# Optimization experiments

Hardware: AMD Instinct MI355X
Metric: run time of the kernel (lower is better)

## Reference

```python
import jax, jax.numpy as jnp
import numpy as np

K = 7            # kernel_size
PAD = 3          # (dilation*(K-1)+1)//2
SHARE = 8        # share_planes
CIN = 512; REL = 64; COUT = 512
B = 4; H = 32; W = 32
EPS = 1e-5


def _patches(x, k, pad):
    """Reflect-pad then extract kxk local windows.
    x: [B,C,H,W] -> [B, C, k*k, H*W] (row-major kernel-offset ordering,
    matching torch Unfold / SAN's Subtraction ordering)."""
    b, c, h, w = x.shape
    xp = jnp.pad(x, ((0, 0), (0, 0), (pad, pad), (pad, pad)), mode='reflect')
    pats = jnp.stack([xp[:, :, i:i + h, j:j + w]
                      for i in range(k) for j in range(k)], axis=2)
    return pats.reshape(b, c, k * k, h * w)


def setup_inputs() -> dict:
    key = jax.random.key(0)
    ks = jax.random.split(key, 16)
    n = lambda k_, shp, s=0.05: jax.random.normal(k_, shp, dtype=jnp.float32) * s
    return {
        'x': jax.random.normal(ks[0], (B, CIN, H, W), dtype=jnp.float32),
        # 1x1 query/key/value projections
        'w1': n(ks[1], (REL, CIN)), 'b1': n(ks[2], (REL,)),
        'w2': n(ks[3], (REL, CIN)), 'b2': n(ks[4], (REL,)),
        'w3': n(ks[5], (COUT, CIN)), 'b3': n(ks[6], (COUT,)),
        # conv_p: 1x1 conv on 2-channel position map
        'wp': n(ks[7], (2, 2), 0.5), 'bp': n(ks[8], (2,)),
        # conv_w: BN(rel+2) -> ReLU -> 1x1(rel+2->rel, no bias) -> BN(rel) -> ReLU -> 1x1(rel->out/share)
        'g0': jnp.ones((REL + 2,), jnp.float32), 'be0': jnp.zeros((REL + 2,), jnp.float32),
        'm0': n(ks[9], (REL + 2,), 0.1),
        'v0': jax.random.uniform(ks[10], (REL + 2,), jnp.float32, 0.5, 1.5),
        'wcw1': n(ks[11], (REL, REL + 2)),
        'g1': jnp.ones((REL,), jnp.float32), 'be1': jnp.zeros((REL,), jnp.float32),
        'm1': n(ks[12], (REL,), 0.1),
        'v1': jax.random.uniform(ks[13], (REL,), jnp.float32, 0.5, 1.5),
        'wcw2': n(ks[14], (COUT // SHARE, REL)), 'bcw2': n(ks[15], (COUT // SHARE,)),
    }


def reference(x, w1, b1, w2, b2, w3, b3, wp, bp,
              g0, be0, m0, v0, wcw1, g1, be1, m1, v1, wcw2, bcw2):
    b, c, h, w = x.shape
    hw = h * w
    conv1x1 = lambda W_, B_, t: jnp.einsum('oc,bchw->bohw', W_, t) + B_[None, :, None, None]
    bn = lambda t, g, be, m, v: ((t - m[None, :, None, None])
                                 * (g * jax.lax.rsqrt(v + EPS))[None, :, None, None]
                                 + be[None, :, None, None])

    x1 = conv1x1(w1, b1, x)   # [B,REL,H,W]
    x2 = conv1x1(w2, b2, x)   # [B,REL,H,W]
    x3 = conv1x1(w3, b3, x)   # [B,COUT,H,W]

    # position map: channel 0 = loc_w, channel 1 = loc_h (as in source)
    lw = jnp.broadcast_to(jnp.linspace(-1.0, 1.0, w)[None, :], (h, w))
    lh = jnp.broadcast_to(jnp.linspace(-1.0, 1.0, h)[:, None], (h, w))
    p = jnp.stack([lw, lh])[None].astype(x.dtype)          # [1,2,H,W]
    p = jnp.einsum('oc,bchw->bohw', wp, p) + bp[None, :, None, None]

    # Subtraction2(x1, x2): center query minus key neighbors -> [B,REL,K*K,HW]
    sub2 = x1.reshape(b, REL, 1, hw) - _patches(x2, K, PAD)
    # Subtraction(p): center minus neighbors -> [1,2,K*K,HW], repeat over batch
    subp = p.reshape(1, 2, 1, hw) - _patches(p, K, PAD)
    subp = jnp.broadcast_to(subp, (b, 2, K * K, hw))

    t = jnp.concatenate([sub2, subp], axis=1)              # [B,REL+2,K*K,HW]
    t = jax.nn.relu(bn(t, g0, be0, m0, v0))
    t = jnp.einsum('oc,bckn->bokn', wcw1, t)               # [B,REL,K*K,HW]
    t = jax.nn.relu(bn(t, g1, be1, m1, v1))
    wgt = jnp.einsum('oc,bckn->bokn', wcw2, t) + bcw2[None, :, None, None]
    wgt = jax.nn.softmax(wgt, axis=-2)                     # softmax over K*K window dim

    # Aggregation: out[b,c,n] = sum_k wgt[b, c//SHARE, k, n] * x3_patch[b,c,k,n]
    x3p = _patches(x3, K, PAD).reshape(b, COUT // SHARE, SHARE, K * K, hw)
    out = jnp.einsum('bgskn,bgkn->bgsn', x3p, wgt)
    return out.reshape(b, COUT, h, w)
```

## Files before the change

### kernel.cpp

```cpp
#include <hip/hip_runtime.h>
#include <hip/hip_bf16.h>
#include <math.h>

typedef float f32x4 __attribute__((ext_vector_type(4)));
typedef short s16x8 __attribute__((ext_vector_type(8)));

#define KKW 49
#define HWTOT 1024
#define CIN 512
#define COUT 512

#define OFF_X1T 0
#define OFF_X2T 262144
#define OFF_X3T 524288
#define OFF_PM  2621440
#define OFF_A0  2623488
#define OFF_C0  2623554
#define OFF_W64 2623620
#define OFF_W65 2623684
#define OFF_C1V 2623748
#define OFF_W1B 2623812
#define OFF_W2B 2625860
#define OFF_W2F 2627908
#define OFF_WT  2629956
#define OFF_XT  2793796
#define WS_NEED_FLOATS 3842372ull

#define SWZ(bb)  ((bb) ^ ((((bb) >> 7) & 7) << 4))

#define GLD16(g, l) __builtin_amdgcn_global_load_lds( \
    (const __attribute__((address_space(1))) void*)(g), \
    (__attribute__((address_space(3))) void*)(l), 16, 0, 0)

__device__ __forceinline__ int refl(int m) {
    if (m < 0) m = -m;
    if (m > 31) m = 62 - m;
    return m;
}

__device__ __forceinline__ unsigned short fbf(float f) {
    unsigned u = __builtin_bit_cast(unsigned, f);
    unsigned r = u + 0x7fffu + ((u >> 16) & 1u);
    return (unsigned short)(r >> 16);
}

__device__ __forceinline__ unsigned pk2bf(float a, float b) {
    float2 f2; f2.x = a; f2.y = b;
    __hip_bfloat162 h = __float22bfloat162_rn(f2);
    union { __hip_bfloat162 h2; unsigned u; } cv;
    cv.h2 = h;
    return cv.u;
}

__device__ __forceinline__ float bf2f(unsigned short u) {
    unsigned v = (unsigned)u << 16;
    return __builtin_bit_cast(float, v);
}

__device__ __forceinline__ void setup_body(
        int tid,
        const float* __restrict__ wp, const float* __restrict__ bp,
        const float* __restrict__ g0, const float* __restrict__ be0,
        const float* __restrict__ m0, const float* __restrict__ v0,
        const float* __restrict__ wcw1,
        const float* __restrict__ g1, const float* __restrict__ be1,
        const float* __restrict__ m1, const float* __restrict__ v1,
        const float* __restrict__ wcw2,
        float* __restrict__ ws) {
    float* pm = ws + OFF_PM;
    for (int n = tid; n < HWTOT; n += 256) {
        int xx = n & 31, yy = n >> 5;
        float lw = -1.f + (2.f / 31.f) * xx;
        float lh = -1.f + (2.f / 31.f) * yy;
        pm[n * 2 + 0] = wp[0] * lw + wp[1] * lh + bp[0];
        pm[n * 2 + 1] = wp[2] * lw + wp[3] * lh + bp[1];
    }
    if (tid < 66) {
        float a = g0[tid] * rsqrtf(v0[tid] + 1e-5f);
        ws[OFF_A0 + tid] = a;
        ws[OFF_C0 + tid] = be0[tid] - m0[tid] * a;
    }
    if (tid < 64) {
        float a1c = g1[tid] * rsqrtf(v1[tid] + 1e-5f);
        ws[OFF_W64 + tid] = a1c * wcw1[tid * 66 + 64];
        ws[OFF_W65 + tid] = a1c * wcw1[tid * 66 + 65];
        ws[OFF_C1V + tid] = be1[tid] - m1[tid] * a1c;
    }
    unsigned short* w1b = (unsigned short*)(ws + OFF_W1B);
    unsigned short* w2f = (unsigned short*)(ws + OFF_W2F);
    for (int t = tid; t < 4096; t += 256) {
        int co = t >> 6, r = t & 63;
        float a1c = g1[co] * rsqrtf(v1[co] + 1e-5f);
        w1b[t] = fbf(a1c * wcw1[co * 66 + r]);
        int j = t & 7, idx = t >> 3;
        int ft = idx >> 6, l = idx & 63;
        int gt = ft >> 1, ks2 = ft & 1;
        int g = (l & 15) + gt * 16;
        int c2 = ks2 * 32 + (l >> 4) * 8 + j;
        w2f[t] = fbf(wcw2[g * 64 + c2]);
    }
}

__global__ void k_setup(const float* __restrict__ wp, const float* __restrict__ bp,
                        const float* __restrict__ g0, const float* __restrict__ be0,
                        const float* __restrict__ m0, const float* __restrict__ v0,
                        const float* __restrict__ wcw1,
                        const float* __restrict__ g1, const float* __restrict__ be1,
                        const float* __restrict__ m1, const float* __restrict__ v1,
                        const float* __restrict__ wcw2,
                        float* __restrict__ ws) {
    setup_body(threadIdx.x, wp, bp, g0, be0, m0, v0, wcw1, g1, be1, m1, v1, wcw2, ws);
}

__global__ __launch_bounds__(256) void k_prep(
        const float* __restrict__ x,
        const float* __restrict__ w1, const float* __restrict__ w2,
        const float* __restrict__ w3,
        const float* __restrict__ wp, const float* __restrict__ bp,
        const float* __restrict__ g0, const float* __restrict__ be0,
        const float* __restrict__ m0, const float* __restrict__ v0,
        const float* __restrict__ wcw1,
        const float* __restrict__ g1, const float* __restrict__ be1,
        const float* __restrict__ m1, const float* __restrict__ v1,
        const float* __restrict__ wcw2,
        float* __restrict__ ws) {
    int bid = blockIdx.x;
    int tid = threadIdx.x;
    if (bid == 296) {
        setup_body(tid, wp, bp, g0, be0, m0, v0, wcw1, g1, be1, m1, v1, wcw2, ws);
    } else if (bid < 40) {
        int mT = bid / 8, kT = bid % 8;
        char* dst = (char*)(ws + OFF_WT) + (mT * 8 + kT) * 16384;
#pragma unroll
        for (int it = 0; it < 4; ++it) {
            int item = it * 256 + tid;
            int m = item >> 3, k8 = item & 7;
            int mg = mT * 128 + m;
            const float* src;
            if (mg < 64) src = w1 + mg * CIN;
            else if (mg < 128) src = w2 + (mg - 64) * CIN;
            else src = w3 + (mg - 128) * CIN;
            int k0 = kT * 64 + k8 * 8;
            s16x8 h;
#pragma unroll
            for (int i = 0; i < 8; i++) h[i] = (short)fbf(src[k0 + i]);
            *(s16x8*)(dst + SWZ(m * 128 + k8 * 16)) = h;
        }
    } else {
        __shared__ float lds[64 * 129];
        int t = bid - 40;
        int b = t >> 6, nT = (t >> 3) & 7, kT = t & 7;
        const float* src = x + (b * CIN + kT * 64) * HWTOT + nT * 128;
#pragma unroll
        for (int it = 0; it < 8; ++it) {
            int item = it * 256 + tid;
            int kk = item >> 5, n4 = item & 31;
            float4 v = *(const float4*)(src + kk * HWTOT + n4 * 4);
            float* d = &lds[kk * 129 + n4 * 4];
            d[0] = v.x; d[1] = v.y; d[2] = v.z; d[3] = v.w;
        }
        __syncthreads();
        char* dst = (char*)(ws + OFF_XT) + ((b * 8 + nT) * 8 + kT) * 16384;
#pragma unroll
        for (int it = 0; it < 4; ++it) {
            int item = it * 256 + tid;
            int n = item >> 3, k8 = item & 7;
            s16x8 h;
#pragma unroll
            for (int i = 0; i < 8; i++) h[i] = (short)fbf(lds[(k8 * 8 + i) * 129 + n]);
            *(s16x8*)(dst + SWZ(n * 128 + k8 * 16)) = h;
        }
    }
}

__global__ __launch_bounds__(256) void k_projm(
        const float* __restrict__ b1, const float* __restrict__ b2,
        const float* __restrict__ b3, float* __restrict__ ws) {
    __shared__ __align__(16) char smem[65536];
    int tid = threadIdx.x, lane = tid & 63, wv = tid >> 6;
    int lidx = lane & 15, q = lane >> 4;
    int mT = blockIdx.x, nT = blockIdx.y, b = blockIdx.z;
    int mh = wv >> 1, nh = wv & 1;
    const char* wtg = (const char*)(ws + OFF_WT) + mT * 8 * 16384;
    const char* xtg = (const char*)(ws + OFF_XT) + (b * 8 + nT) * 8 * 16384;

    f32x4 acc[4][4];
#pragma unroll
    for (int i = 0; i < 4; i++)
#pragma unroll
        for (int j = 0; j < 4; j++) acc[i][j] = (f32x4)0.f;

#define STAGE(kt, buf) do { \
        const char* ga_ = wtg + (kt) * 16384; \
        const char* gb_ = xtg + (kt) * 16384; \
        char* la_ = smem + (buf) * 32768; \
        char* lb_ = la_ + 16384; \
        _Pragma("unroll") \
        for (int c_ = 0; c_ < 4; c_++) { \
            GLD16(ga_ + c_ * 4096 + wv * 1024 + lane * 16, la_ + c_ * 4096 + wv * 1024); \
            GLD16(gb_ + c_ * 4096 + wv * 1024 + lane * 16, lb_ + c_ * 4096 + wv * 1024); \
        } \
    } while (0)

    STAGE(0, 0);
    __syncthreads();
    for (int kt = 0; kt < 8; kt++) {
        if (kt < 7) STAGE(kt + 1, (kt + 1) & 1);
        const char* la = smem + (kt & 1) * 32768;
        const char* lb = la + 16384;
#pragma unroll
        for (int ks = 0; ks < 2; ks++) {
            s16x8 af[4], bf[4];
            int kb = ks * 64 + q * 16;
#pragma unroll
            for (int f = 0; f < 4; f++) {
                int arow = mh * 64 + f * 16 + lidx;
                int brow = nh * 64 + f * 16 + lidx;
                af[f] = *(const s16x8*)(la + SWZ(arow * 128 + kb));
                bf[f] = *(const s16x8*)(lb + SWZ(brow * 128 + kb));
            }
#pragma unroll
            for (int mf = 0; mf < 4; mf++)
#pragma unroll
                for (int nf = 0; nf < 4; nf++)
                    acc[mf][nf] = __builtin_amdgcn_mfma_f32_16x16x32_bf16(
                        af[mf], bf[nf], acc[mf][nf], 0, 0, 0);
        }
        __syncthreads();
    }
#undef STAGE

    unsigned short* x1t = (unsigned short*)(ws + OFF_X1T);
    unsigned short* x2t = (unsigned short*)(ws + OFF_X2T);
    unsigned short* x3t = (unsigned short*)(ws + OFF_X3T);
#pragma unroll
    for (int mf = 0; mf < 4; mf++) {
        int mloc = mh * 64 + mf * 16 + q * 4;
        int mg = mT * 128 + mloc;
#pragma unroll
        for (int nf = 0; nf < 4; nf++) {
            int n = nT * 128 + nh * 64 + nf * 16 + lidx;
            float o[4];
            uint2 pk;
            if (mg < 64) {
#pragma unroll
                for (int r = 0; r < 4; r++)
                    o[r] = ws[OFF_A0 + mg + r] * (acc[mf][nf][r] + b1[mg + r]) + ws[OFF_C0 + mg + r];
                pk.x = pk2bf(o[0], o[1]); pk.y = pk2bf(o[2], o[3]);
                *(uint2*)(x1t + (size_t)(b * HWTOT + n) * 64 + mg) = pk;
            } else if (mg < 128) {
                int c = mg - 64;
#pragma unroll
                for (int r = 0; r < 4; r++)
                    o[r] = ws[OFF_A0 + c + r] * (acc[mf][nf][r] + b2[c + r]);
                pk.x = pk2bf(o[0], o[1]); pk.y = pk2bf(o[2], o[3]);
                *(uint2*)(x2t + (size_t)(b * HWTOT + n) * 64 + c) = pk;
            } else {
                int c = mg - 128;
#pragma unroll
                for (int r = 0; r < 4; r++)
                    o[r] = acc[mf][nf][r] + b3[c + r];
                pk.x = pk2bf(o[0], o[1]); pk.y = pk2bf(o[2], o[3]);
                *(uint2*)(x3t + (size_t)(b * HWTOT + n) * 512 + c) = pk;
            }
        }
    }
}

__global__ __launch_bounds__(256) void k_proj(
        const float* __restrict__ x,
        const float* __restrict__ w1, const float* __restrict__ b1,
        const float* __restrict__ w2, const float* __restrict__ b2,
        const float* __restrict__ w3, const float* __restrict__ b3,
        float* __restrict__ ws) {
    __shared__ __align__(16) float As[64 * 17];
    __shared__ __align__(16) float Bs[16 * 64];
    int tid = threadIdx.x;
    int n0 = blockIdx.x * 64;
    int mT = blockIdx.y;
    int b = blockIdx.z;
    int mq = tid >> 4, nq = tid & 15;
    float acc[4][4];
#pragma unroll
    for (int i = 0; i < 4; i++)
#pragma unroll
        for (int j = 0; j < 4; j++) acc[i][j] = 0.f;

    for (int k0 = 0; k0 < CIN; k0 += 16) {
#pragma unroll
        for (int i = 0; i < 4; i++) {
            int t = tid + i * 256;
            int k = t & 15, m = t >> 4;
            int mg = mT * 64 + m;
            const float* Wrow;
            if (mg < 64) Wrow = w1 + mg * CIN;
            else if (mg < 128) Wrow = w2 + (mg - 64) * CIN;
            else Wrow = w3 + (mg - 128) * CIN;
            As[m * 17 + k] = Wrow[k0 + k];
        }
#pragma unroll
        for (int i = 0; i < 4; i++) {
            int t = tid + i * 256;
            int n = t & 63, k = t >> 6;
            Bs[k * 64 + n] = x[(b * CIN + k0 + k) * HWTOT + n0 + n];
        }
        __syncthreads();
#pragma unroll
        for (int k = 0; k < 16; k++) {
            float4 bv = *(const float4*)&Bs[k * 64 + nq * 4];
            float av[4];
#pragma unroll
            for (int i = 0; i < 4; i++) av[i] = As[(mq * 4 + i) * 17 + k];
#pragma unroll
            for (int i = 0; i < 4; i++) {
                acc[i][0] += av[i] * bv.x;
                acc[i][1] += av[i] * bv.y;
                acc[i][2] += av[i] * bv.z;
                acc[i][3] += av[i] * bv.w;
            }
        }
        __syncthreads();
    }
    unsigned short* x1t = (unsigned short*)(ws + OFF_X1T);
    unsigned short* x2t = (unsigned short*)(ws + OFF_X2T);
    unsigned short* x3t = (unsigned short*)(ws + OFF_X3T);
#pragma unroll
    for (int i = 0; i < 4; i++) {
        int mg = mT * 64 + mq * 4 + i;
        if (mg < 64) {
            float bias = b1[mg];
            float aa = ws[OFF_A0 + mg], cc = ws[OFF_C0 + mg];
#pragma unroll
            for (int j = 0; j < 4; j++) {
                int n = n0 + nq * 4 + j;
                x1t[(size_t)(b * HWTOT + n) * 64 + mg] = fbf(aa * (acc[i][j] + bias) + cc);
            }
        } else if (mg < 128) {
            int r = mg - 64;
            float bias = b2[r];
            float aa = ws[OFF_A0 + r];
#pragma unroll
            for (int j = 0; j < 4; j++) {
                int n = n0 + nq * 4 + j;
                x2t[(size_t)(b * HWTOT + n) * 64 + r] = fbf(aa * (acc[i][j] + bias));
            }
        } else {
            float bias = b3[mg - 128];
#pragma unroll
            for (int j = 0; j < 4; j++) {
                int n = n0 + nq * 4 + j;
                x3t[(size_t)(b * HWTOT + n) * 512 + (mg - 128)] = fbf(acc[i][j] + bias);
            }
        }
    }
}

__global__ __launch_bounds__(64, 4) void k_fused(
        const float* __restrict__ ws, float* __restrict__ out) {
    __shared__ __align__(16) char smem[8960];

    int lane = threadIdx.x;
    int lidx = lane & 15;
    int q = lane >> 4;

    int bid = blockIdx.x;
    int p = (bid & 7) * 512 + (bid >> 3);
    int b = p >> 10;
    int n = p & 1023;
    int y = n >> 5, x0 = n & 31;

    char* t1p = smem;
    float* auxf = (float*)(smem + 8192);
    int* nbo = (int*)(smem + 8704);

    const unsigned short* x1t = (const unsigned short*)(ws + OFF_X1T);
    const unsigned short* x2t = (const unsigned short*)(ws + OFF_X2T);
    const unsigned short* x3t = (const unsigned short*)(ws + OFF_X3T);
    const float* pm  = ws + OFF_PM;
    const unsigned short* w1b = (const unsigned short*)(ws + OFF_W1B);
    const unsigned short* w2f = (const unsigned short*)(ws + OFF_W2F);

    {
        int k = lane;
        int di = k / 7 - 3, dj = k % 7 - 3;
        int nb = refl(y + di) * 32 + refl(x0 + dj);
        nbo[k] = nb;
        float a064 = ws[OFF_A0 + 64], c064 = ws[OFF_C0 + 64];
        float a065 = ws[OFF_A0 + 65], c065 = ws[OFF_C0 + 65];
        auxf[k]      = fmaxf(fmaf(a064, pm[n * 2 + 0] - pm[nb * 2 + 0], c064), 0.f);
        auxf[64 + k] = fmaxf(fmaf(a065, pm[n * 2 + 1] - pm[nb * 2 + 1], c065), 0.f);
    }
    asm volatile("s_waitcnt lgkmcnt(0)" ::: "memory");
    __builtin_amdgcn_sched_barrier(0);

    s16x8 af1[4][2];
#pragma unroll
    for (int cot = 0; cot < 4; cot++)
#pragma unroll
        for (int ks = 0; ks < 2; ks++)
            af1[cot][ks] = *(const s16x8*)(w1b + (lidx + 16 * cot) * 64 + ks * 32 + q * 8);

    const unsigned short* x1r = x1t + (size_t)(b * HWTOT + n) * 64 + q * 8;
    float x1f[2][8];
    {
        s16x8 h0 = *(const s16x8*)(x1r);
        s16x8 h1 = *(const s16x8*)(x1r + 32);
#pragma unroll
        for (int i = 0; i < 8; i++) {
            x1f[0][i] = bf2f((unsigned short)h0[i]);
            x1f[1][i] = bf2f((unsigned short)h1[i]);
        }
    }

#pragma unroll
    for (int ct = 0; ct < 4; ct++) {
        int col = lidx + 16 * ct;
        int nb = nbo[col];
        const unsigned short* x2r = x2t + (size_t)(b * HWTOT + nb) * 64 + q * 8;
        f32x4 acc1[4];
#pragma unroll
        for (int cot = 0; cot < 4; cot++) acc1[cot] = (f32x4)0.f;
#pragma unroll
        for (int ks = 0; ks < 2; ks++) {
            s16x8 v = *(const s16x8*)(x2r + ks * 32);
            union { s16x8 v; unsigned u[4]; } bb;
#pragma unroll
            for (int w = 0; w < 4; w++)
                bb.u[w] = pk2bf(
                    fmaxf(x1f[ks][2 * w]     - bf2f((unsigned short)v[2 * w]),     0.f),
                    fmaxf(x1f[ks][2 * w + 1] - bf2f((unsigned short)v[2 * w + 1]), 0.f));
#pragma unroll
            for (int cot = 0; cot < 4; cot++)
                acc1[cot] = __builtin_amdgcn_mfma_f32_16x16x32_bf16(af1[cot][ks], bb.v, acc1[cot], 0, 0, 0);
        }
        float s64 = auxf[col], s65 = auxf[64 + col];
#pragma unroll
        for (int cot = 0; cot < 4; cot++) {
            f32x4 wa = *(const f32x4*)(ws + OFF_W64 + cot * 16 + q * 4);
            f32x4 wb = *(const f32x4*)(ws + OFF_W65 + cot * 16 + q * 4);
            f32x4 cc = *(const f32x4*)(ws + OFF_C1V + cot * 16 + q * 4);
            float t[4];
#pragma unroll
            for (int r = 0; r < 4; r++)
                t[r] = fmaxf(acc1[cot][r] + wa[r] * s64 + wb[r] * s65 + cc[r], 0.f);
            uint2 pk;
            pk.x = pk2bf(t[0], t[1]);
            pk.y = pk2bf(t[2], t[3]);
            int byte = col * 128 + cot * 32 + q * 8;
            *(uint2*)(t1p + SWZ(byte)) = pk;
        }
    }

    asm volatile("s_waitcnt lgkmcnt(0)" ::: "memory");
    __builtin_amdgcn_sched_barrier(0);

    s16x8 af2[4][2];
#pragma unroll
    for (int gt = 0; gt < 4; gt++)
#pragma unroll
        for (int ks2 = 0; ks2 < 2; ks2++)
            af2[gt][ks2] = *(const s16x8*)(w2f + ((gt * 2 + ks2) * 64 + lane) * 8);

    unsigned held[4][4][2];
#pragma unroll
    for (int gt = 0; gt < 4; gt++) {
        f32x4 acc2[4];
#pragma unroll
        for (int kt = 0; kt < 4; kt++) acc2[kt] = (f32x4)0.f;
#pragma unroll
        for (int kt = 0; kt < 4; kt++) {
#pragma unroll
            for (int ks2 = 0; ks2 < 2; ks2++) {
                int byte = (lidx + 16 * kt) * 128 + ks2 * 64 + q * 16;
                s16x8 a = *(const s16x8*)(t1p + SWZ(byte));
                acc2[kt] = __builtin_amdgcn_mfma_f32_16x16x32_bf16(a, af2[gt][ks2], acc2[kt], 0, 0, 0);
            }
        }
        float mx = -1e30f;
#pragma unroll
        for (int kt = 0; kt < 3; kt++)
#pragma unroll
            for (int r = 0; r < 4; r++) mx = fmaxf(mx, acc2[kt][r]);
        if (q == 0) mx = fmaxf(mx, acc2[3][0]);
        mx = fmaxf(mx, __shfl_xor(mx, 16));
        mx = fmaxf(mx, __shfl_xor(mx, 32));
        float e[4][4];
        float sum = 0.f;
#pragma unroll
        for (int kt = 0; kt < 4; kt++)
#pragma unroll
            for (int r = 0; r < 4; r++) {
                bool valid = (kt < 3) || (q == 0 && r == 0);
                float ev = valid ? exp2f((acc2[kt][r] - mx) * 1.44269504f) : 0.f;
                e[kt][r] = ev;
                sum += ev;
            }
        sum += __shfl_xor(sum, 16);
        sum += __shfl_xor(sum, 32);
        float inv = 1.f / sum;
#pragma unroll
        for (int kt = 0; kt < 4; kt++) {
            held[gt][kt][0] = pk2bf(e[kt][0] * inv, e[kt][1] * inv);
            held[gt][kt][1] = pk2bf(e[kt][2] * inv, e[kt][3] * inv);
        }
    }

#pragma unroll
    for (int gt = 0; gt < 4; gt++)
#pragma unroll
        for (int kt = 0; kt < 4; kt++) {
            int byte = (lidx + 16 * gt) * 128 + kt * 32 + q * 8;
            uint2 pk;
            pk.x = held[gt][kt][0];
            pk.y = held[gt][kt][1];
            *(uint2*)(t1p + SWZ(byte)) = pk;
        }

    asm volatile("s_waitcnt lgkmcnt(0)" ::: "memory");
    __builtin_amdgcn_sched_barrier(0);

    s16x8 wrow[7];
#pragma unroll
    for (int i = 0; i < 7; i++)
        wrow[i] = *(const s16x8*)(t1p + SWZ(lane * 128 + i * 16));

    f32x4 a30 = (f32x4)0.f, a31 = (f32x4)0.f;
    const unsigned short* x3b = x3t + (size_t)b * HWTOT * 512 + lane * 8;
#pragma unroll
    for (int k = 0; k < KKW; k++) {
        int nb = nbo[k];
        float w = bf2f((unsigned short)wrow[k >> 3][k & 7]);
        s16x8 v = *(const s16x8*)(x3b + (size_t)nb * 512);
#pragma unroll
        for (int r = 0; r < 4; r++) {
            a30[r] = fmaf(w, bf2f((unsigned short)v[r]), a30[r]);
            a31[r] = fmaf(w, bf2f((unsigned short)v[4 + r]), a31[r]);
        }
    }
    float* ob = out + ((size_t)b * COUT + lane * 8) * HWTOT + n;
#pragma unroll
    for (int i = 0; i < 4; i++) ob[i * HWTOT] = a30[i];
#pragma unroll
    for (int i = 0; i < 4; i++) ob[(i + 4) * HWTOT] = a31[i];
}

extern "C" void kernel_launch(void* const* d_in, const int* in_sizes, int n_in,
                              void* d_out, int out_size, void* d_ws, size_t ws_size,
                              hipStream_t stream) {
    const float* x = (const float*)d_in[0];
    const float* w1 = (const float*)d_in[1];
    const float* b1 = (const float*)d_in[2];
    const float* w2 = (const float*)d_in[3];
    const float* b2 = (const float*)d_in[4];
    const float* w3 = (const float*)d_in[5];
    const float* b3 = (const float*)d_in[6];
    const float* wp = (const float*)d_in[7];
    const float* bp = (const float*)d_in[8];
    const float* g0 = (const float*)d_in[9];
    const float* be0 = (const float*)d_in[10];
    const float* m0 = (const float*)d_in[11];
    const float* v0 = (const float*)d_in[12];
    const float* wcw1 = (const float*)d_in[13];
    const float* g1 = (const float*)d_in[14];
    const float* be1 = (const float*)d_in[15];
    const float* m1 = (const float*)d_in[16];
    const float* v1 = (const float*)d_in[17];
    const float* wcw2 = (const float*)d_in[18];
    float* ws = (float*)d_ws;
    float* out = (float*)d_out;

    if (ws_size >= WS_NEED_FLOATS * 4ull) {
        k_prep<<<297, 256, 0, stream>>>(x, w1, w2, w3, wp, bp, g0, be0, m0, v0,
                                        wcw1, g1, be1, m1, v1, wcw2, ws);
        k_projm<<<dim3(5, 8, 4), 256, 0, stream>>>(b1, b2, b3, ws);
    } else {
        k_setup<<<1, 256, 0, stream>>>(wp, bp, g0, be0, m0, v0, wcw1, g1, be1, m1, v1, wcw2, ws);
        k_proj<<<dim3(16, 10, 4), 256, 0, stream>>>(x, w1, b1, w2, b2, w3, b3, ws);
    }
    k_fused<<<4096, 64, 0, stream>>>(ws, out);
}
```

Baseline: 62.33 us.

## Split fused attention kernel into weight-compute and aggregation kernels

```diff
diff --git a/kernel.cpp b/kernel.cpp
--- a/kernel.cpp
+++ b/kernel.cpp
@@ -25,6 +25,8 @@
 #define OFF_WT  2629956
 #define OFF_XT  2793796
 #define WS_NEED_FLOATS 3842372ull
+#define OFF_WGT 3842372
+#define WS_SPLIT_FLOATS 12230980ull
 
 #define SWZ(bb)  ((bb) ^ ((((bb) >> 7) & 7) << 4))
 
@@ -352,6 +354,240 @@
                 x3t[(size_t)(b * HWTOT + n) * 512 + (mg - 128)] = fbf(acc[i][j] + bias);
             }
         }
+    }
+}
+
+__global__ __launch_bounds__(64, 4) void k_attn(float* __restrict__ ws) {
+    __shared__ __align__(16) char smem[8960];
+
+    int lane = threadIdx.x;
+    int lidx = lane & 15;
+    int q = lane >> 4;
+
+    int bid = blockIdx.x;
+    int p = (bid & 7) * 512 + (bid >> 3);
+    int b = p >> 10;
+    int n = p & 1023;
+    int y = n >> 5, x0 = n & 31;
+
+    char* t1p = smem;
+    float* auxf = (float*)(smem + 8192);
+    int* nbo = (int*)(smem + 8704);
+
+    const unsigned short* x1t = (const unsigned short*)(ws + OFF_X1T);
+    const unsigned short* x2t = (const unsigned short*)(ws + OFF_X2T);
+    const float* pm  = ws + OFF_PM;
+    const unsigned short* w1b = (const unsigned short*)(ws + OFF_W1B);
+    const unsigned short* w2f = (const unsigned short*)(ws + OFF_W2F);
+
+    {
+        int k = lane;
+        int di = k / 7 - 3, dj = k % 7 - 3;
+        int nb = refl(y + di) * 32 + refl(x0 + dj);
+        nbo[k] = nb;
+        float a064 = ws[OFF_A0 + 64], c064 = ws[OFF_C0 + 64];
+        float a065 = ws[OFF_A0 + 65], c065 = ws[OFF_C0 + 65];
+        auxf[k]      = fmaxf(fmaf(a064, pm[n * 2 + 0] - pm[nb * 2 + 0], c064), 0.f);
+        auxf[64 + k] = fmaxf(fmaf(a065, pm[n * 2 + 1] - pm[nb * 2 + 1], c065), 0.f);
+    }
+    asm volatile("s_waitcnt lgkmcnt(0)" ::: "memory");
+    __builtin_amdgcn_sched_barrier(0);
+
+    s16x8 af1[4][2];
+#pragma unroll
+    for (int cot = 0; cot < 4; cot++)
+#pragma unroll
+        for (int ks = 0; ks < 2; ks++)
+            af1[cot][ks] = *(const s16x8*)(w1b + (lidx + 16 * cot) * 64 + ks * 32 + q * 8);
+
+    int nbv[4];
+#pragma unroll
+    for (int ct = 0; ct < 4; ct++) nbv[ct] = nbo[lidx + 16 * ct];
+
+    s16x8 xv[4][2];
+#pragma unroll
+    for (int ct = 0; ct < 4; ct++) {
+        const unsigned short* x2r = x2t + (size_t)(b * HWTOT + nbv[ct]) * 64 + q * 8;
+        xv[ct][0] = *(const s16x8*)(x2r);
+        xv[ct][1] = *(const s16x8*)(x2r + 32);
+    }
+
+    const unsigned short* x1r = x1t + (size_t)(b * HWTOT + n) * 64 + q * 8;
+    float x1f[2][8];
+    {
+        s16x8 h0 = *(const s16x8*)(x1r);
+        s16x8 h1 = *(const s16x8*)(x1r + 32);
+#pragma unroll
+        for (int i = 0; i < 8; i++) {
+            x1f[0][i] = bf2f((unsigned short)h0[i]);
+            x1f[1][i] = bf2f((unsigned short)h1[i]);
+        }
+    }
+
+#pragma unroll
+    for (int ct = 0; ct < 4; ct++) {
+        int col = lidx + 16 * ct;
+        f32x4 acc1[4];
+#pragma unroll
+        for (int cot = 0; cot < 4; cot++) acc1[cot] = (f32x4)0.f;
+#pragma unroll
+        for (int ks = 0; ks < 2; ks++) {
+            s16x8 v = xv[ct][ks];
+            union { s16x8 v; unsigned u[4]; } bb;
+#pragma unroll
+            for (int w = 0; w < 4; w++)
+                bb.u[w] = pk2bf(
+                    fmaxf(x1f[ks][2 * w]     - bf2f((unsigned short)v[2 * w]),     0.f),
+                    fmaxf(x1f[ks][2 * w + 1] - bf2f((unsigned short)v[2 * w + 1]), 0.f));
+#pragma unroll
+            for (int cot = 0; cot < 4; cot++)
+                acc1[cot] = __builtin_amdgcn_mfma_f32_16x16x32_bf16(af1[cot][ks], bb.v, acc1[cot], 0, 0, 0);
+        }
+        float s64 = auxf[col], s65 = auxf[64 + col];
+#pragma unroll
+        for (int cot = 0; cot < 4; cot++) {
+            f32x4 wa = *(const f32x4*)(ws + OFF_W64 + cot * 16 + q * 4);
+            f32x4 wb = *(const f32x4*)(ws + OFF_W65 + cot * 16 + q * 4);
+            f32x4 cc = *(const f32x4*)(ws + OFF_C1V + cot * 16 + q * 4);
+            float t[4];
+#pragma unroll
+            for (int r = 0; r < 4; r++)
+                t[r] = fmaxf(acc1[cot][r] + wa[r] * s64 + wb[r] * s65 + cc[r], 0.f);
+            uint2 pk;
+            pk.x = pk2bf(t[0], t[1]);
+            pk.y = pk2bf(t[2], t[3]);
+            int byte = col * 128 + cot * 32 + q * 8;
+            *(uint2*)(t1p + SWZ(byte)) = pk;
+        }
+    }
+
+    asm volatile("s_waitcnt lgkmcnt(0)" ::: "memory");
+    __builtin_amdgcn_sched_barrier(0);
+
+    char* wgtp = (char*)(ws + OFF_WGT) + (size_t)p * 8192;
+#pragma unroll
+    for (int gt = 0; gt < 4; gt++) {
+        s16x8 af2[2];
+#pragma unroll
+        for (int ks2 = 0; ks2 < 2; ks2++)
+            af2[ks2] = *(const s16x8*)(w2f + ((gt * 2 + ks2) * 64 + lane) * 8);
+        f32x4 acc2[4];
+#pragma unroll
+        for (int kt = 0; kt < 4; kt++) acc2[kt] = (f32x4)0.f;
+#pragma unroll
+        for (int kt = 0; kt < 4; kt++) {
+#pragma unroll
+            for (int ks2 = 0; ks2 < 2; ks2++) {
+                int byte = (lidx + 16 * kt) * 128 + ks2 * 64 + q * 16;
+                s16x8 a = *(const s16x8*)(t1p + SWZ(byte));
+                acc2[kt] = __builtin_amdgcn_mfma_f32_16x16x32_bf16(a, af2[ks2], acc2[kt], 0, 0, 0);
+            }
+        }
+        float mx = -1e30f;
+#pragma unroll
+        for (int kt = 0; kt < 3; kt++)
+#pragma unroll
+            for (int r = 0; r < 4; r++) mx = fmaxf(mx, acc2[kt][r]);
+        if (q == 0) mx = fmaxf(mx, acc2[3][0]);
+        mx = fmaxf(mx, __shfl_xor(mx, 16));
+        mx = fmaxf(mx, __shfl_xor(mx, 32));
+        float e[4][4];
+        float sum = 0.f;
+#pragma unroll
+        for (int kt = 0; kt < 4; kt++)
+#pragma unroll
+            for (int r = 0; r < 4; r++) {
+                bool valid = (kt < 3) || (q == 0 && r == 0);
+                float ev = valid ? exp2f((acc2[kt][r] - mx) * 1.44269504f) : 0.f;
+                e[kt][r] = ev;
+                sum += ev;
+            }
+        sum += __shfl_xor(sum, 16);
+        sum += __shfl_xor(sum, 32);
+        float inv = 1.f / sum;
+#pragma unroll
+        for (int kt = 0; kt < 4; kt++) {
+            uint2 pk;
+            pk.x = pk2bf(e[kt][0] * inv, e[kt][1] * inv);
+            pk.y = pk2bf(e[kt][2] * inv, e[kt][3] * inv);
+            *(uint2*)(wgtp + (lidx + 16 * gt) * 128 + kt * 32 + q * 8) = pk;
+        }
+    }
+}
+
+__global__ __launch_bounds__(64, 4) void k_agg(
+        const float* __restrict__ ws, float* __restrict__ out) {
+    __shared__ int nboL[64];
+    int lane = threadIdx.x;
+    int bid = blockIdx.x;
+    int idx = (bid & 7) * 256 + (bid >> 3);
+    int p0 = idx * 2;
+    int b = p0 >> 10;
+    int n = p0 & 1023;
+    int y = n >> 5, x0 = n & 31;
+
+    if (lane < 56) {
+        int dy = lane >> 3, dxp = lane & 7;
+        nboL[lane] = refl(y + dy - 3) * 32 + refl(x0 + dxp - 3);
+    }
+    asm volatile("s_waitcnt lgkmcnt(0)" ::: "memory");
+    __builtin_amdgcn_sched_barrier(0);
+
+    const unsigned short* wgt = (const unsigned short*)(ws + OFF_WGT);
+    const unsigned short* w0p = wgt + (size_t)p0 * 4096 + lane * 64;
+    s16x8 w0[7], w1[7];
+#pragma unroll
+    for (int i = 0; i < 7; i++) {
+        w0[i] = *(const s16x8*)(w0p + i * 8);
+        w1[i] = *(const s16x8*)(w0p + 4096 + i * 8);
+    }
+
+    const unsigned short* x3b = (const unsigned short*)(ws + OFF_X3T)
+                              + (size_t)b * HWTOT * 512 + lane * 8;
+    f32x4 a00 = (f32x4)0.f, a01 = (f32x4)0.f;
+    f32x4 a10 = (f32x4)0.f, a11 = (f32x4)0.f;
+
+    s16x8 vb[4];
+#pragma unroll
+    for (int i = 0; i < 4; i++)
+        vb[i] = *(const s16x8*)(x3b + (size_t)nboL[i] * 512);
+
+#pragma unroll
+    for (int i = 0; i < 56; i++) {
+        s16x8 v = vb[i & 3];
+        if (i + 4 < 56)
+            vb[i & 3] = *(const s16x8*)(x3b + (size_t)nboL[i + 4] * 512);
+        int dy = i >> 3, dxp = i & 7;
+        if (dxp < 7) {
+            int k0 = dy * 7 + dxp;
+            float w = bf2f((unsigned short)w0[k0 >> 3][k0 & 7]);
+#pragma unroll
+            for (int r = 0; r < 4; r++) {
+                a00[r] = fmaf(w, bf2f((unsigned short)v[r]), a00[r]);
+                a01[r] = fmaf(w, bf2f((unsigned short)v[4 + r]), a01[r]);
+            }
+        }
+        if (dxp > 0) {
+            int k1 = dy * 7 + dxp - 1;
+            float w = bf2f((unsigned short)w1[k1 >> 3][k1 & 7]);
+#pragma unroll
+            for (int r = 0; r < 4; r++) {
+                a10[r] = fmaf(w, bf2f((unsigned short)v[r]), a10[r]);
+                a11[r] = fmaf(w, bf2f((unsigned short)v[4 + r]), a11[r]);
+            }
+        }
+    }
+
+    float* ob = out + ((size_t)b * COUT + lane * 8) * HWTOT + n;
+#pragma unroll
+    for (int i = 0; i < 4; i++) {
+        float2 t; t.x = a00[i]; t.y = a10[i];
+        *(float2*)(ob + (size_t)i * HWTOT) = t;
+    }
+#pragma unroll
+    for (int i = 0; i < 4; i++) {
+        float2 t; t.x = a01[i]; t.y = a11[i];
+        *(float2*)(ob + (size_t)(i + 4) * HWTOT) = t;
     }
 }
 
@@ -577,5 +813,10 @@
         k_setup<<<1, 256, 0, stream>>>(wp, bp, g0, be0, m0, v0, wcw1, g1, be1, m1, v1, wcw2, ws);
         k_proj<<<dim3(16, 10, 4), 256, 0, stream>>>(x, w1, b1, w2, b2, w3, b3, ws);
     }
-    k_fused<<<4096, 64, 0, stream>>>(ws, out);
-}
+    if (ws_size >= WS_SPLIT_FLOATS * 4ull) {
+        k_attn<<<4096, 64, 0, stream>>>(ws);
+        k_agg<<<2048, 64, 0, stream>>>(ws, out);
+    } else {
+        k_fused<<<4096, 64, 0, stream>>>(ws, out);
+    }
+}
```

Result: slower. 236.0 us (+278.7%).

## Halve projection GEMM N-tile for more blocks; prefetch neighbor loads in fused kernel

Applied to the files above, without the earlier changes.

```diff
diff --git a/kernel.cpp b/kernel.cpp
--- a/kernel.cpp
+++ b/kernel.cpp
@@ -176,51 +176,55 @@
 __global__ __launch_bounds__(256) void k_projm(
         const float* __restrict__ b1, const float* __restrict__ b2,
         const float* __restrict__ b3, float* __restrict__ ws) {
-    __shared__ __align__(16) char smem[65536];
+    __shared__ __align__(16) char smem[49152];
     int tid = threadIdx.x, lane = tid & 63, wv = tid >> 6;
     int lidx = lane & 15, q = lane >> 4;
-    int mT = blockIdx.x, nT = blockIdx.y, b = blockIdx.z;
-    int mh = wv >> 1, nh = wv & 1;
+    int mT = blockIdx.x, nTT = blockIdx.y, b = blockIdx.z;
+    int nT = nTT >> 1, nHalf = nTT & 1;
     const char* wtg = (const char*)(ws + OFF_WT) + mT * 8 * 16384;
     const char* xtg = (const char*)(ws + OFF_XT) + (b * 8 + nT) * 8 * 16384;
 
-    f32x4 acc[4][4];
-#pragma unroll
-    for (int i = 0; i < 4; i++)
+    f32x4 acc[2][4];
+#pragma unroll
+    for (int i = 0; i < 2; i++)
 #pragma unroll
         for (int j = 0; j < 4; j++) acc[i][j] = (f32x4)0.f;
 
 #define STAGE(kt, buf) do { \
         const char* ga_ = wtg + (kt) * 16384; \
-        const char* gb_ = xtg + (kt) * 16384; \
-        char* la_ = smem + (buf) * 32768; \
+        const char* gb_ = xtg + (kt) * 16384 + nHalf * 8192; \
+        char* la_ = smem + (buf) * 24576; \
         char* lb_ = la_ + 16384; \
         _Pragma("unroll") \
-        for (int c_ = 0; c_ < 4; c_++) { \
+        for (int c_ = 0; c_ < 4; c_++) \
             GLD16(ga_ + c_ * 4096 + wv * 1024 + lane * 16, la_ + c_ * 4096 + wv * 1024); \
+        _Pragma("unroll") \
+        for (int c_ = 0; c_ < 2; c_++) \
             GLD16(gb_ + c_ * 4096 + wv * 1024 + lane * 16, lb_ + c_ * 4096 + wv * 1024); \
-        } \
     } while (0)
 
     STAGE(0, 0);
     __syncthreads();
     for (int kt = 0; kt < 8; kt++) {
         if (kt < 7) STAGE(kt + 1, (kt + 1) & 1);
-        const char* la = smem + (kt & 1) * 32768;
+        const char* la = smem + (kt & 1) * 24576;
         const char* lb = la + 16384;
 #pragma unroll
         for (int ks = 0; ks < 2; ks++) {
-            s16x8 af[4], bf[4];
+            s16x8 af[2], bf[4];
             int kb = ks * 64 + q * 16;
 #pragma unroll
+            for (int f = 0; f < 2; f++) {
+                int arow = wv * 32 + f * 16 + lidx;
+                af[f] = *(const s16x8*)(la + SWZ(arow * 128 + kb));
+            }
+#pragma unroll
             for (int f = 0; f < 4; f++) {
-                int arow = mh * 64 + f * 16 + lidx;
-                int brow = nh * 64 + f * 16 + lidx;
-                af[f] = *(const s16x8*)(la + SWZ(arow * 128 + kb));
+                int brow = f * 16 + lidx;
                 bf[f] = *(const s16x8*)(lb + SWZ(brow * 128 + kb));
             }
 #pragma unroll
-            for (int mf = 0; mf < 4; mf++)
+            for (int mf = 0; mf < 2; mf++)
 #pragma unroll
                 for (int nf = 0; nf < 4; nf++)
                     acc[mf][nf] = __builtin_amdgcn_mfma_f32_16x16x32_bf16(
@@ -234,12 +238,12 @@
     unsigned short* x2t = (unsigned short*)(ws + OFF_X2T);
     unsigned short* x3t = (unsigned short*)(ws + OFF_X3T);
 #pragma unroll
-    for (int mf = 0; mf < 4; mf++) {
-        int mloc = mh * 64 + mf * 16 + q * 4;
+    for (int mf = 0; mf < 2; mf++) {
+        int mloc = wv * 32 + mf * 16 + q * 4;
         int mg = mT * 128 + mloc;
 #pragma unroll
         for (int nf = 0; nf < 4; nf++) {
-            int n = nT * 128 + nh * 64 + nf * 16 + lidx;
+            int n = nTT * 64 + nf * 16 + lidx;
             float o[4];
             uint2 pk;
             if (mg < 64) {
@@ -357,7 +361,7 @@
 
 __global__ __launch_bounds__(64, 4) void k_fused(
         const float* __restrict__ ws, float* __restrict__ out) {
-    __shared__ __align__(16) char smem[8960];
+    __shared__ __align__(16) char smem[8448];
 
     int lane = threadIdx.x;
     int lidx = lane & 15;
@@ -370,8 +374,7 @@
     int y = n >> 5, x0 = n & 31;
 
     char* t1p = smem;
-    float* auxf = (float*)(smem + 8192);
-    int* nbo = (int*)(smem + 8704);
+    int* nbo = (int*)(smem + 8192);
 
     const unsigned short* x1t = (const unsigned short*)(ws + OFF_X1T);
     const unsigned short* x2t = (const unsigned short*)(ws + OFF_X2T);
@@ -381,17 +384,27 @@
     const unsigned short* w2f = (const unsigned short*)(ws + OFF_W2F);
 
     {
-        int k = lane;
-        int di = k / 7 - 3, dj = k % 7 - 3;
+        int di = lane / 7 - 3, dj = lane % 7 - 3;
+        nbo[lane] = refl(y + di) * 32 + refl(x0 + dj);
+    }
+
+    float pmn0 = pm[n * 2], pmn1 = pm[n * 2 + 1];
+    float a064 = ws[OFF_A0 + 64], c064 = ws[OFF_C0 + 64];
+    float a065 = ws[OFF_A0 + 65], c065 = ws[OFF_C0 + 65];
+    float s64v[4], s65v[4];
+    s16x8 xv[4][2];
+#pragma unroll
+    for (int ct = 0; ct < 4; ct++) {
+        int col = lidx + 16 * ct;
+        int di = col / 7 - 3, dj = col % 7 - 3;
         int nb = refl(y + di) * 32 + refl(x0 + dj);
-        nbo[k] = nb;
-        float a064 = ws[OFF_A0 + 64], c064 = ws[OFF_C0 + 64];
-        float a065 = ws[OFF_A0 + 65], c065 = ws[OFF_C0 + 65];
-        auxf[k]      = fmaxf(fmaf(a064, pm[n * 2 + 0] - pm[nb * 2 + 0], c064), 0.f);
-        auxf[64 + k] = fmaxf(fmaf(a065, pm[n * 2 + 1] - pm[nb * 2 + 1], c065), 0.f);
-    }
-    asm volatile("s_waitcnt lgkmcnt(0)" ::: "memory");
-    __builtin_amdgcn_sched_barrier(0);
+        const unsigned short* x2r = x2t + (size_t)(b * HWTOT + nb) * 64 + q * 8;
+        xv[ct][0] = *(const s16x8*)(x2r);
+        xv[ct][1] = *(const s16x8*)(x2r + 32);
+        float2 pmb = *(const float2*)(pm + nb * 2);
+        s64v[ct] = fmaxf(fmaf(a064, pmn0 - pmb.x, c064), 0.f);
+        s65v[ct] = fmaxf(fmaf(a065, pmn1 - pmb.y, c065), 0.f);
+    }
 
     s16x8 af1[4][2];
 #pragma unroll
@@ -415,14 +428,12 @@
 #pragma unroll
     for (int ct = 0; ct < 4; ct++) {
         int col = lidx + 16 * ct;
-        int nb = nbo[col];
-        const unsigned short* x2r = x2t + (size_t)(b * HWTOT + nb) * 64 + q * 8;
         f32x4 acc1[4];
 #pragma unroll
         for (int cot = 0; cot < 4; cot++) acc1[cot] = (f32x4)0.f;
 #pragma unroll
         for (int ks = 0; ks < 2; ks++) {
-            s16x8 v = *(const s16x8*)(x2r + ks * 32);
+            s16x8 v = xv[ct][ks];
             union { s16x8 v; unsigned u[4]; } bb;
 #pragma unroll
             for (int w = 0; w < 4; w++)
@@ -433,7 +444,6 @@
             for (int cot = 0; cot < 4; cot++)
                 acc1[cot] = __builtin_amdgcn_mfma_f32_16x16x32_bf16(af1[cot][ks], bb.v, acc1[cot], 0, 0, 0);
         }
-        float s64 = auxf[col], s65 = auxf[64 + col];
 #pragma unroll
         for (int cot = 0; cot < 4; cot++) {
             f32x4 wa = *(const f32x4*)(ws + OFF_W64 + cot * 16 + q * 4);
@@ -442,7 +452,7 @@
             float t[4];
 #pragma unroll
             for (int r = 0; r < 4; r++)
-                t[r] = fmaxf(acc1[cot][r] + wa[r] * s64 + wb[r] * s65 + cc[r], 0.f);
+                t[r] = fmaxf(acc1[cot][r] + wa[r] * s64v[ct] + wb[r] * s65v[ct] + cc[r], 0.f);
             uint2 pk;
             pk.x = pk2bf(t[0], t[1]);
             pk.y = pk2bf(t[2], t[3]);
@@ -572,7 +582,7 @@
     if (ws_size >= WS_NEED_FLOATS * 4ull) {
         k_prep<<<297, 256, 0, stream>>>(x, w1, w2, w3, wp, bp, g0, be0, m0, v0,
                                         wcw1, g1, be1, m1, v1, wcw2, ws);
-        k_projm<<<dim3(5, 8, 4), 256, 0, stream>>>(b1, b2, b3, ws);
+        k_projm<<<dim3(5, 16, 4), 256, 0, stream>>>(b1, b2, b3, ws);
     } else {
         k_setup<<<1, 256, 0, stream>>>(wp, bp, g0, be0, m0, v0, wcw1, g1, be1, m1, v1, wcw2, ws);
         k_proj<<<dim3(16, 10, 4), 256, 0, stream>>>(x, w1, b1, w2, b2, w3, b3, ws);
```

Measured after the change: 58.46 us. -6.2%, faster.
